# Performance work log

Measured on AMD Instinct MI355X. Metric: run time of the kernel, lower is better.

## Reference

```python
import jax, jax.numpy as jnp
import numpy as np

NH = 12      # bert-base heads
NL = 32      # num_latents
K = 64       # hard-coded topk in forward


def _ln(x, g, b):
    m = x.mean(-1, keepdims=True)
    v = ((x - m) ** 2).mean(-1, keepdims=True)
    return (x - m) / jnp.sqrt(v + 1e-12) * g + b


def _attn(xq, xkv, w, b, mask_add=None):
    # w: [4,H,H] (q,k,v,o), b: [4,H]
    B, Lq, H = xq.shape
    dh = H // NH
    q = (xq @ w[0] + b[0]).reshape(B, Lq, NH, dh)
    k = (xkv @ w[1] + b[1]).reshape(B, -1, NH, dh)
    v = (xkv @ w[2] + b[2]).reshape(B, -1, NH, dh)
    s = jnp.einsum('bqhd,bkhd->bhqk', q, k) / np.sqrt(dh).astype(xq.dtype)
    if mask_add is not None:
        s = s + mask_add
    p = jax.nn.softmax(s, axis=-1)          # [B,NH,Lq,Lk]
    o = jnp.einsum('bhqk,bkhd->bqhd', p, v).reshape(B, Lq, H)
    return o @ w[3] + b[3], p


def _cross_block(q, enc, w, b, g, lb, mask_add=None):
    # w:[L,8,H,H]; per layer: self-attn+LN then cross-attn+LN (FFN stripped)
    p_last = None
    for l in range(w.shape[0]):
        a, _ = _attn(q, q, w[l, :4], b[l, :4])
        q = _ln(q + a, g[l, 0], lb[l, 0])
        a, p_last = _attn(q, enc, w[l, 4:], b[l, 4:], mask_add)
        q = _ln(q + a, g[l, 1], lb[l, 1])
    return q, p_last


def _self_block(q, w, b, g, lb):
    probs = []
    for l in range(w.shape[0]):
        a, p = _attn(q, q, w[l], b[l])
        q = _ln(q + a, g[l, 0], lb[l, 0])
        probs.append(p)
    return q, jnp.concatenate(probs, axis=1)  # concat over head dim like torch.concat(attentions, dim=1)


def setup_inputs() -> dict:
    key = jax.random.key(0)
    ks = jax.random.split(key, 24)
    B, S, T, H, L = 32, 1024, 64, 768, 2
    std = 0.02
    inp = {
        'audio_embeds': jax.random.normal(ks[0], (B, S, H), jnp.float32),
        'text_embeds': jax.random.normal(ks[1], (B, T, H), jnp.float32),
        'attention_mask': jnp.ones((B, T), jnp.int32),
        'audio_qt': jax.random.normal(ks[2], (1, NL, H), jnp.float32) * std,
        'text_qt': jax.random.normal(ks[3], (1, NL, H), jnp.float32) * std,
    }
    for i, pre in enumerate(['tm', 'am', 'mg']):
        inp[pre + '_w'] = jax.random.normal(ks[4 + i], (L, 8, H, H), jnp.float32) * std
        inp[pre + '_b'] = jnp.zeros((L, 8, H), jnp.float32)
        inp[pre + '_g'] = jnp.ones((L, 2, H), jnp.float32)
        inp[pre + '_lb'] = jnp.zeros((L, 2, H), jnp.float32)
    inp['sel_w'] = jax.random.normal(ks[8], (L, 4, H, H), jnp.float32) * std
    inp['sel_b'] = jnp.zeros((L, 4, H), jnp.float32)
    inp['sel_g'] = jnp.ones((L, 1, H), jnp.float32)
    inp['sel_lb'] = jnp.zeros((L, 1, H), jnp.float32)
    return inp


def reference(audio_embeds, text_embeds, audio_qt, text_qt,
              tm_w, tm_b, tm_g, tm_lb, am_w, am_b, am_g, am_lb,
              sel_w, sel_b, sel_g, sel_lb, mg_w, mg_b, mg_g, mg_lb,
              attention_mask):
    B, S, H = audio_embeds.shape
    mask_add = (1.0 - attention_mask.astype(audio_embeds.dtype))[:, None, None, :] * -1e4

    # text token merger
    latent_text, _ = _cross_block(jnp.broadcast_to(text_qt, (B, NL, H)), text_embeds,
                                  tm_w, tm_b, tm_g, tm_lb, mask_add)
    # audio token merger (capture last-layer cross-attn probs)
    latent_audio, cross_p = _cross_block(jnp.broadcast_to(audio_qt, (B, NL, H)), audio_embeds,
                                         am_w, am_b, am_g, am_lb)
    latent_attention_score = cross_p.mean(axis=1)          # [B,NL,S]

    latent = jnp.concatenate([latent_audio, latent_text], axis=1)  # [B,2NL,H]
    fused, attn_all = _self_block(latent, sel_w, sel_b, sel_g, sel_lb)  # attn_all [B,L*NH,2NL,2NL]
    aas = attn_all[:, :, :NL, NL:].mean(axis=1)            # [B,NL,NL]

    imp = jnp.einsum('bqk,bks->bqs', aas, latent_attention_score).mean(axis=1)  # [B,S]
    _, idx = jax.lax.top_k(imp, K)
    sorted_idx = jnp.sort(idx, axis=1)                     # [B,K]

    sel_mask = jnp.zeros((B, S), bool).at[jnp.arange(B)[:, None], sorted_idx].set(True)
    q_tokens = jnp.take_along_axis(audio_embeds, sorted_idx[..., None], axis=1)  # [B,K,H]
    unsel_idx = jnp.argsort(sel_mask, axis=1, stable=True)[:, :S - K]            # order-preserving
    kv_rest = jnp.take_along_axis(audio_embeds, unsel_idx[..., None], axis=1)    # [B,S-K,H]
    kv = jnp.concatenate([kv_rest, fused], axis=1)                               # [B,S,H]

    out, _ = _cross_block(q_tokens, kv, mg_w, mg_b, mg_g, mg_lb)
    return out
```

## Files before the change

### kernel.cpp

```cpp
#include <hip/hip_runtime.h>
#include <hip/hip_bf16.h>
#include <math.h>

namespace {
constexpr int kB = 32, kS = 1024, kT = 64, kH = 768, kNH = 12, kDH = 64;
constexpr int kNL = 32, kTopK = 64, kL = 2;
constexpr size_t kMat = (size_t)kH * kH;
}

typedef _Float16 half8 __attribute__((ext_vector_type(8)));
typedef float floatx4 __attribute__((ext_vector_type(4)));

#define AS1U(p) ((const __attribute__((address_space(1))) unsigned int*)(p))
#define AS3U(p) ((__attribute__((address_space(3))) unsigned int*)(p))

__device__ __forceinline__ void split_write(float v, _Float16* H, _Float16* L, size_t i) {
    _Float16 h = (_Float16)v;
    H[i] = h;
    L[i] = (_Float16)(v - (float)h);
}

template<int NP>
__global__ __launch_bounds__(256) void gemm16(
    const _Float16* __restrict__ Aqh, const _Float16* __restrict__ Aql,
    const _Float16* __restrict__ Aeh, const _Float16* __restrict__ Ael,
    const _Float16* __restrict__ Whb, const _Float16* __restrict__ Wlb,
    const float* __restrict__ bias,
    _Float16* __restrict__ O0h, _Float16* __restrict__ O0l,
    _Float16* __restrict__ O1h, _Float16* __restrict__ O1l,
    _Float16* __restrict__ O2h, _Float16* __restrict__ O2l,
    int Mq, int Mk)
{
    const int z = blockIdx.z;
    const int M = (z == 0) ? Mq : Mk;
    if ((int)blockIdx.x * 128 >= M) return;
    const _Float16* Ah = (z == 0) ? Aqh : Aeh;
    const _Float16* Al = (z == 0) ? Aql : Ael;
    const _Float16* Bh = Whb + (size_t)z * kMat;
    const _Float16* Bl = Wlb + (size_t)z * kMat;
    const float* bz = bias + z * kH;
    _Float16* Oh = (z == 0) ? O0h : (z == 1) ? O1h : O2h;
    _Float16* Ol = (z == 0) ? O0l : (z == 1) ? O1l : O2l;

    constexpr int NPL = (NP == 3) ? 4 : 2;
    __shared__ _Float16 lds[NPL * 4096];
    const int tid = threadIdx.x;
    const int lane = tid & 63, wave = tid >> 6;
    const size_t rm = (size_t)blockIdx.x * 128;
    const size_t cn = (size_t)blockIdx.y * 128;
    const int wr = (wave >> 1) * 64, wc = (wave & 1) * 64;

    const int lrow = lane >> 2;
    const int lchunk = (lane & 3) ^ ((lane >> 3) & 3);
    const int q = lane >> 4;
    const int fr = lane & 15;
    const int rslot = q ^ ((fr >> 1) & 3);

    const _Float16* gsrc;
    _Float16* lbase;
    int jbase;
    if constexpr (NP == 3) {
        gsrc = (wave == 0) ? Ah + rm * kH : (wave == 1) ? Al + rm * kH
             : (wave == 2) ? Bh + cn * kH : Bl + cn * kH;
        lbase = &lds[wave * 4096];
        jbase = 0;
    } else {
        gsrc = (wave < 2) ? Ah + rm * kH : Bh + cn * kH;
        lbase = &lds[(wave >> 1) * 4096];
        jbase = (wave & 1) * 4;
    }
    constexpr int CPW = (NP == 3) ? 8 : 4;

    floatx4 acc[4][4] = {};

    for (int k0 = 0; k0 < kH; k0 += 32) {
        #pragma unroll
        for (int c = 0; c < CPW; ++c) {
            int j = jbase + c;
            const _Float16* src = gsrc + (size_t)(j * 16 + lrow) * kH + k0 + lchunk * 8;
            _Float16* dst = lbase + j * 512 + lane * 8;
            __builtin_amdgcn_global_load_lds(AS1U(src), AS3U(dst), 16, 0, 0);
        }
        __syncthreads();

        half8 ah[4], bh[4], al[4], bl[4];
        #pragma unroll
        for (int m = 0; m < 4; ++m) {
            int r = wr + m * 16 + fr;
            ah[m] = *(const half8*)&lds[r * 32 + rslot * 8];
            if constexpr (NP == 3) al[m] = *(const half8*)&lds[4096 + r * 32 + rslot * 8];
        }
        constexpr int pb = (NP == 3) ? 2 : 1;
        #pragma unroll
        for (int n = 0; n < 4; ++n) {
            int r = wc + n * 16 + fr;
            bh[n] = *(const half8*)&lds[pb * 4096 + r * 32 + rslot * 8];
            if constexpr (NP == 3) bl[n] = *(const half8*)&lds[3 * 4096 + r * 32 + rslot * 8];
        }
        #pragma unroll
        for (int m = 0; m < 4; ++m)
            #pragma unroll
            for (int n = 0; n < 4; ++n) {
                acc[m][n] = __builtin_amdgcn_mfma_f32_16x16x32_f16(ah[m], bh[n], acc[m][n], 0, 0, 0);
                if constexpr (NP == 3) {
                    acc[m][n] = __builtin_amdgcn_mfma_f32_16x16x32_f16(ah[m], bl[n], acc[m][n], 0, 0, 0);
                    acc[m][n] = __builtin_amdgcn_mfma_f32_16x16x32_f16(al[m], bh[n], acc[m][n], 0, 0, 0);
                }
            }
        __syncthreads();
    }
    #pragma unroll
    for (int m = 0; m < 4; ++m) {
        int row0 = wr + m * 16 + (lane >> 4) * 4;
        #pragma unroll
        for (int n = 0; n < 4; ++n) {
            int col = (int)cn + wc + n * 16 + fr;
            float bv = bz[col];
            #pragma unroll
            for (int j = 0; j < 4; ++j) {
                float v = acc[m][n][j] + bv;
                size_t oi = (rm + row0 + j) * (size_t)kH + col;
                _Float16 hh = (_Float16)v;
                Oh[oi] = hh;
                if constexpr (NP == 3) Ol[oi] = (_Float16)(v - (float)hh);
            }
        }
    }
}

template<int NP>
__global__ __launch_bounds__(256) void gemm16s(
    const _Float16* __restrict__ Aqh, const _Float16* __restrict__ Aql,
    const _Float16* __restrict__ Aeh, const _Float16* __restrict__ Ael,
    const _Float16* __restrict__ Whb, const _Float16* __restrict__ Wlb,
    const float* __restrict__ bias,
    _Float16* __restrict__ O0h, _Float16* __restrict__ O0l,
    _Float16* __restrict__ O1h, _Float16* __restrict__ O1l,
    _Float16* __restrict__ O2h, _Float16* __restrict__ O2l,
    int Mq, int Mk)
{
    const int z = blockIdx.z;
    const int M = (z == 0) ? Mq : Mk;
    if ((int)blockIdx.x * 64 >= M) return;
    const _Float16* Ah = (z == 0) ? Aqh : Aeh;
    const _Float16* Al = (z == 0) ? Aql : Ael;
    const _Float16* Bh = Whb + (size_t)z * kMat;
    const _Float16* Bl = Wlb + (size_t)z * kMat;
    const float* bz = bias + z * kH;
    _Float16* Oh = (z == 0) ? O0h : (z == 1) ? O1h : O2h;
    _Float16* Ol = (z == 0) ? O0l : (z == 1) ? O1l : O2l;

    constexpr int NPL = (NP == 3) ? 4 : 2;
    __shared__ _Float16 lds[NPL * 2048];
    const int tid = threadIdx.x;
    const int lane = tid & 63, wave = tid >> 6;
    const size_t rm = (size_t)blockIdx.x * 64;
    const size_t cn = (size_t)blockIdx.y * 64;
    const int wr = (wave >> 1) * 32, wc = (wave & 1) * 32;

    const int lrow = lane >> 2;
    const int lchunk = (lane & 3) ^ ((lane >> 3) & 3);
    const int q = lane >> 4;
    const int fr = lane & 15;
    const int rslot = q ^ ((fr >> 1) & 3);

    const _Float16* gsrc;
    _Float16* lbase;
    int jbase;
    if constexpr (NP == 3) {
        gsrc = (wave == 0) ? Ah + rm * kH : (wave == 1) ? Al + rm * kH
             : (wave == 2) ? Bh + cn * kH : Bl + cn * kH;
        lbase = &lds[wave * 2048];
        jbase = 0;
    } else {
        gsrc = (wave < 2) ? Ah + rm * kH : Bh + cn * kH;
        lbase = &lds[(wave >> 1) * 2048];
        jbase = (wave & 1) * 2;
    }
    constexpr int CPW = (NP == 3) ? 4 : 2;

    floatx4 acc[2][2] = {};

    for (int k0 = 0; k0 < kH; k0 += 32) {
        #pragma unroll
        for (int c = 0; c < CPW; ++c) {
            int j = jbase + c;
            const _Float16* src = gsrc + (size_t)(j * 16 + lrow) * kH + k0 + lchunk * 8;
            _Float16* dst = lbase + j * 512 + lane * 8;
            __builtin_amdgcn_global_load_lds(AS1U(src), AS3U(dst), 16, 0, 0);
        }
        __syncthreads();

        half8 ah[2], bh[2], al[2], bl[2];
        #pragma unroll
        for (int m = 0; m < 2; ++m) {
            int r = wr + m * 16 + fr;
            ah[m] = *(const half8*)&lds[r * 32 + rslot * 8];
            if constexpr (NP == 3) al[m] = *(const half8*)&lds[2048 + r * 32 + rslot * 8];
        }
        constexpr int pb = (NP == 3) ? 2 : 1;
        #pragma unroll
        for (int n = 0; n < 2; ++n) {
            int r = wc + n * 16 + fr;
            bh[n] = *(const half8*)&lds[pb * 2048 + r * 32 + rslot * 8];
            if constexpr (NP == 3) bl[n] = *(const half8*)&lds[3 * 2048 + r * 32 + rslot * 8];
        }
        #pragma unroll
        for (int m = 0; m < 2; ++m)
            #pragma unroll
            for (int n = 0; n < 2; ++n) {
                acc[m][n] = __builtin_amdgcn_mfma_f32_16x16x32_f16(ah[m], bh[n], acc[m][n], 0, 0, 0);
                if constexpr (NP == 3) {
                    acc[m][n] = __builtin_amdgcn_mfma_f32_16x16x32_f16(ah[m], bl[n], acc[m][n], 0, 0, 0);
                    acc[m][n] = __builtin_amdgcn_mfma_f32_16x16x32_f16(al[m], bh[n], acc[m][n], 0, 0, 0);
                }
            }
        __syncthreads();
    }
    #pragma unroll
    for (int m = 0; m < 2; ++m) {
        int row0 = wr + m * 16 + (lane >> 4) * 4;
        #pragma unroll
        for (int n = 0; n < 2; ++n) {
            int col = (int)cn + wc + n * 16 + fr;
            float bv = bz[col];
            #pragma unroll
            for (int j = 0; j < 4; ++j) {
                float v = acc[m][n][j] + bv;
                size_t oi = (rm + row0 + j) * (size_t)kH + col;
                _Float16 hh = (_Float16)v;
                Oh[oi] = hh;
                if constexpr (NP == 3) Ol[oi] = (_Float16)(v - (float)hh);
            }
        }
    }
}

template<int NP>
__global__ __launch_bounds__(256) void gemm_o32s(
    const _Float16* __restrict__ Ah_, const _Float16* __restrict__ Al_,
    const _Float16* __restrict__ Bh_, const _Float16* __restrict__ Bl_,
    const float* __restrict__ bias, float* __restrict__ Y, int M)
{
    constexpr int NPL = (NP == 3) ? 4 : 2;
    __shared__ _Float16 lds[NPL * 2048];
    const int tid = threadIdx.x;
    const int lane = tid & 63, wave = tid >> 6;
    const size_t rm = (size_t)blockIdx.x * 64;
    const size_t cn = (size_t)blockIdx.y * 64;
    const int wr = (wave >> 1) * 32, wc = (wave & 1) * 32;

    const int lrow = lane >> 2;
    const int lchunk = (lane & 3) ^ ((lane >> 3) & 3);
    const int q = lane >> 4;
    const int fr = lane & 15;
    const int rslot = q ^ ((fr >> 1) & 3);

    const _Float16* gsrc;
    _Float16* lbase;
    int jbase;
    if constexpr (NP == 3) {
        gsrc = (wave == 0) ? Ah_ + rm * kH : (wave == 1) ? Al_ + rm * kH
             : (wave == 2) ? Bh_ + cn * kH : Bl_ + cn * kH;
        lbase = &lds[wave * 2048];
        jbase = 0;
    } else {
        gsrc = (wave < 2) ? Ah_ + rm * kH : Bh_ + cn * kH;
        lbase = &lds[(wave >> 1) * 2048];
        jbase = (wave & 1) * 2;
    }
    constexpr int CPW = (NP == 3) ? 4 : 2;

    floatx4 acc[2][2] = {};
    for (int k0 = 0; k0 < kH; k0 += 32) {
        #pragma unroll
        for (int c = 0; c < CPW; ++c) {
            int j = jbase + c;
            const _Float16* src = gsrc + (size_t)(j * 16 + lrow) * kH + k0 + lchunk * 8;
            _Float16* dst = lbase + j * 512 + lane * 8;
            __builtin_amdgcn_global_load_lds(AS1U(src), AS3U(dst), 16, 0, 0);
        }
        __syncthreads();
        half8 ah[2], bh[2], al[2], bl[2];
        #pragma unroll
        for (int m = 0; m < 2; ++m) {
            int r = wr + m * 16 + fr;
            ah[m] = *(const half8*)&lds[r * 32 + rslot * 8];
            if constexpr (NP == 3) al[m] = *(const half8*)&lds[2048 + r * 32 + rslot * 8];
        }
        constexpr int pb = (NP == 3) ? 2 : 1;
        #pragma unroll
        for (int n = 0; n < 2; ++n) {
            int r = wc + n * 16 + fr;
            bh[n] = *(const half8*)&lds[pb * 2048 + r * 32 + rslot * 8];
            if constexpr (NP == 3) bl[n] = *(const half8*)&lds[3 * 2048 + r * 32 + rslot * 8];
        }
        #pragma unroll
        for (int m = 0; m < 2; ++m)
            #pragma unroll
            for (int n = 0; n < 2; ++n) {
                acc[m][n] = __builtin_amdgcn_mfma_f32_16x16x32_f16(ah[m], bh[n], acc[m][n], 0, 0, 0);
                if constexpr (NP == 3) {
                    acc[m][n] = __builtin_amdgcn_mfma_f32_16x16x32_f16(ah[m], bl[n], acc[m][n], 0, 0, 0);
                    acc[m][n] = __builtin_amdgcn_mfma_f32_16x16x32_f16(al[m], bh[n], acc[m][n], 0, 0, 0);
                }
            }
        __syncthreads();
    }
    #pragma unroll
    for (int m = 0; m < 2; ++m) {
        int row0 = wr + m * 16 + (lane >> 4) * 4;
        #pragma unroll
        for (int n = 0; n < 2; ++n) {
            int col = (int)cn + wc + n * 16 + fr;
            float bv = bias[col];
            #pragma unroll
            for (int j = 0; j < 4; ++j)
                Y[(rm + row0 + j) * (size_t)kH + col] = acc[m][n][j] + bv;
        }
    }
}

template<int NP>
__global__ __launch_bounds__(256) void attn_big(
    const _Float16* __restrict__ Qh, const _Float16* __restrict__ Ql,
    const _Float16* __restrict__ Kh, const _Float16* __restrict__ Kl,
    float* __restrict__ P, int Lq, int Lk)
{
    constexpr int NPL = (NP == 3) ? 2 : 1;
    const int tid = threadIdx.x, lane = tid & 63, wave = tid >> 6;
    const int fr = lane & 15, part = lane >> 4;
    const int bh = blockIdx.x, b = bh / kNH, h = bh % kNH;
    const int q0 = blockIdx.y * 32;
    const int key0 = wave * 256;
    __shared__ float red[32][4];

    half8 qa[2][2][NPL];
    #pragma unroll
    for (int m = 0; m < 2; ++m)
        #pragma unroll
        for (int c = 0; c < 2; ++c) {
            size_t ro = (size_t)(b * Lq + q0 + m * 16 + fr) * kH + h * kDH + c * 32 + part * 8;
            qa[m][c][0] = *(const half8*)&Qh[ro];
            if constexpr (NP == 3) qa[m][c][1] = *(const half8*)&Ql[ro];
        }
    floatx4 acc[2][16] = {};
    #pragma unroll
    for (int n = 0; n < 16; ++n)
        #pragma unroll
        for (int c = 0; c < 2; ++c) {
            size_t ro = (size_t)(b * Lk + key0 + n * 16 + fr) * kH + h * kDH + c * 32 + part * 8;
            half8 kh8 = *(const half8*)&Kh[ro];
            half8 kl8;
            if constexpr (NP == 3) kl8 = *(const half8*)&Kl[ro];
            #pragma unroll
            for (int m = 0; m < 2; ++m) {
                acc[m][n] = __builtin_amdgcn_mfma_f32_16x16x32_f16(qa[m][c][0], kh8, acc[m][n], 0, 0, 0);
                if constexpr (NP == 3) {
                    acc[m][n] = __builtin_amdgcn_mfma_f32_16x16x32_f16(qa[m][c][0], kl8, acc[m][n], 0, 0, 0);
                    acc[m][n] = __builtin_amdgcn_mfma_f32_16x16x32_f16(qa[m][c][1], kh8, acc[m][n], 0, 0, 0);
                }
            }
        }
    #pragma unroll
    for (int m = 0; m < 2; ++m)
        #pragma unroll
        for (int n = 0; n < 16; ++n)
            #pragma unroll
            for (int j = 0; j < 4; ++j) acc[m][n][j] *= 0.125f;
    #pragma unroll
    for (int m = 0; m < 2; ++m)
        #pragma unroll
        for (int j = 0; j < 4; ++j) {
            float v = acc[m][0][j];
            #pragma unroll
            for (int n = 1; n < 16; ++n) v = fmaxf(v, acc[m][n][j]);
            #pragma unroll
            for (int o = 1; o < 16; o <<= 1) v = fmaxf(v, __shfl_xor(v, o));
            red[m * 16 + part * 4 + j][wave] = v;
        }
    __syncthreads();
    float gm[2][4];
    #pragma unroll
    for (int m = 0; m < 2; ++m)
        #pragma unroll
        for (int j = 0; j < 4; ++j) {
            int r = m * 16 + part * 4 + j;
            gm[m][j] = fmaxf(fmaxf(red[r][0], red[r][1]), fmaxf(red[r][2], red[r][3]));
        }
    __syncthreads();
    #pragma unroll
    for (int m = 0; m < 2; ++m)
        #pragma unroll
        for (int j = 0; j < 4; ++j) {
            float s = 0.f;
            #pragma unroll
            for (int n = 0; n < 16; ++n) {
                float e = expf(acc[m][n][j] - gm[m][j]);
                acc[m][n][j] = e;
                s += e;
            }
            #pragma unroll
            for (int o = 1; o < 16; o <<= 1) s += __shfl_xor(s, o);
            red[m * 16 + part * 4 + j][wave] = s;
        }
    __syncthreads();
    #pragma unroll
    for (int m = 0; m < 2; ++m)
        #pragma unroll
        for (int j = 0; j < 4; ++j) {
            int r = m * 16 + part * 4 + j;
            float inv = 1.0f / (red[r][0] + red[r][1] + red[r][2] + red[r][3]);
            size_t rowbase = ((size_t)bh * Lq + q0 + m * 16 + part * 4 + j) * Lk + key0;
            #pragma unroll
            for (int n = 0; n < 16; ++n)
                P[rowbase + n * 16 + fr] = acc[m][n][j] * inv;
        }
}

template<int LQ, int NP>
__global__ __launch_bounds__((LQ / 16) * 64) void pv_mfma(
    const float* __restrict__ P,
    const _Float16* __restrict__ Vh, const _Float16* __restrict__ Vl,
    _Float16* __restrict__ Oh, _Float16* __restrict__ Ol, int Lk)
{
    constexpr int NW = LQ / 16, NT = NW * 64;
    constexpr int NPL = (NP == 3) ? 2 : 1;
    __shared__ _Float16 vT[NPL][64][72];
    const int tid = threadIdx.x, lane = tid & 63, wave = tid >> 6;
    const int fr = lane & 15, part = lane >> 4;
    const int bh = blockIdx.x, b = bh / kNH, h = bh % kNH;
    const int qbase = wave * 16;

    floatx4 acc[4] = {};
    for (int kb = 0; kb < Lk; kb += 64) {
        for (int idx = tid; idx < 64 * 8; idx += NT) {
            int r = idx >> 3, c8 = idx & 7;
            half8 v = *(const half8*)&Vh[(size_t)(b * Lk + kb + r) * kH + h * kDH + c8 * 8];
            #pragma unroll
            for (int e = 0; e < 8; ++e) vT[0][c8 * 8 + e][r] = v[e];
            if constexpr (NP == 3) {
                half8 w = *(const half8*)&Vl[(size_t)(b * Lk + kb + r) * kH + h * kDH + c8 * 8];
                #pragma unroll
                for (int e = 0; e < 8; ++e) vT[1][c8 * 8 + e][r] = w[e];
            }
        }
        __syncthreads();
        half8 pa[2][NPL];
        #pragma unroll
        for (int c = 0; c < 2; ++c) {
            const float* src = &P[((size_t)bh * LQ + qbase + fr) * Lk + kb + c * 32 + part * 8];
            float4 x = *(const float4*)src, y = *(const float4*)(src + 4);
            float vv[8] = {x.x, x.y, x.z, x.w, y.x, y.y, y.z, y.w};
            #pragma unroll
            for (int e = 0; e < 8; ++e) {
                _Float16 hh = (_Float16)vv[e];
                pa[c][0][e] = hh;
                if constexpr (NP == 3) pa[c][1][e] = (_Float16)(vv[e] - (float)hh);
            }
        }
        #pragma unroll
        for (int n = 0; n < 4; ++n)
            #pragma unroll
            for (int c = 0; c < 2; ++c) {
                half8 bh8 = *(const half8*)&vT[0][n * 16 + fr][c * 32 + part * 8];
                acc[n] = __builtin_amdgcn_mfma_f32_16x16x32_f16(pa[c][0], bh8, acc[n], 0, 0, 0);
                if constexpr (NP == 3) {
                    half8 bl8 = *(const half8*)&vT[1][n * 16 + fr][c * 32 + part * 8];
                    acc[n] = __builtin_amdgcn_mfma_f32_16x16x32_f16(pa[c][0], bl8, acc[n], 0, 0, 0);
                    acc[n] = __builtin_amdgcn_mfma_f32_16x16x32_f16(pa[c][1], bh8, acc[n], 0, 0, 0);
                }
            }
        __syncthreads();
    }
    #pragma unroll
    for (int n = 0; n < 4; ++n)
        #pragma unroll
        for (int j = 0; j < 4; ++j) {
            size_t oi = (size_t)(b * LQ + qbase + part * 4 + j) * kH + h * kDH + n * 16 + fr;
            float v = acc[n][j];
            _Float16 hh = (_Float16)v;
            Oh[oi] = hh;
            if constexpr (NP == 3) Ol[oi] = (_Float16)(v - (float)hh);
        }
}

template<int LQ, int LK, int NP, bool MASKED, bool CAPTURE>
__global__ __launch_bounds__((LQ / 16) * 64) void attn_small(
    const _Float16* Qh, const _Float16* Ql,
    const _Float16* __restrict__ Kh, const _Float16* __restrict__ Kl,
    const _Float16* __restrict__ Vh, const _Float16* __restrict__ Vl,
    _Float16* Oh, _Float16* Ol,
    float* __restrict__ Pcap, const int* __restrict__ amask)
{
    constexpr int NW = LQ / 16, NT = NW * 64, NN = LK / 16, NC = LK / 32;
    constexpr int NPL = (NP == 3) ? 2 : 1;
    constexpr int PIT = LK + 8;
    __shared__ _Float16 vT[NPL][64][PIT];
    __shared__ _Float16 Pld[NW][NPL][16][PIT];
    const int tid = threadIdx.x, lane = tid & 63, wave = tid >> 6;
    const int fr = lane & 15, part = lane >> 4;
    const int bh = blockIdx.x, b = bh / kNH, h = bh % kNH;

    for (int idx = tid; idx < LK * 8; idx += NT) {
        int r = idx >> 3, c8 = idx & 7;
        half8 v = *(const half8*)&Vh[(size_t)(b * LK + r) * kH + h * kDH + c8 * 8];
        #pragma unroll
        for (int e = 0; e < 8; ++e) vT[0][c8 * 8 + e][r] = v[e];
        if constexpr (NP == 3) {
            half8 w = *(const half8*)&Vl[(size_t)(b * LK + r) * kH + h * kDH + c8 * 8];
            #pragma unroll
            for (int e = 0; e < 8; ++e) vT[1][c8 * 8 + e][r] = w[e];
        }
    }
    half8 qa[2][NPL];
    #pragma unroll
    for (int c = 0; c < 2; ++c) {
        size_t ro = (size_t)(b * LQ + wave * 16 + fr) * kH + h * kDH + c * 32 + part * 8;
        qa[c][0] = *(const half8*)&Qh[ro];
        if constexpr (NP == 3) qa[c][1] = *(const half8*)&Ql[ro];
    }
    floatx4 acc[NN] = {};
    #pragma unroll
    for (int n = 0; n < NN; ++n)
        #pragma unroll
        for (int c = 0; c < 2; ++c) {
            size_t ro = (size_t)(b * LK + n * 16 + fr) * kH + h * kDH + c * 32 + part * 8;
            half8 kh8 = *(const half8*)&Kh[ro];
            acc[n] = __builtin_amdgcn_mfma_f32_16x16x32_f16(qa[c][0], kh8, acc[n], 0, 0, 0);
            if constexpr (NP == 3) {
                half8 kl8 = *(const half8*)&Kl[ro];
                acc[n] = __builtin_amdgcn_mfma_f32_16x16x32_f16(qa[c][0], kl8, acc[n], 0, 0, 0);
                acc[n] = __builtin_amdgcn_mfma_f32_16x16x32_f16(qa[c][1], kh8, acc[n], 0, 0, 0);
            }
        }
    #pragma unroll
    for (int n = 0; n < NN; ++n) {
        float madd = 0.f;
        if constexpr (MASKED)
            madd = (1.0f - (float)amask[b * kT + n * 16 + fr]) * -1e4f;
        #pragma unroll
        for (int j = 0; j < 4; ++j) acc[n][j] = acc[n][j] * 0.125f + madd;
    }
    #pragma unroll
    for (int j = 0; j < 4; ++j) {
        float m = acc[0][j];
        #pragma unroll
        for (int n = 1; n < NN; ++n) m = fmaxf(m, acc[n][j]);
        #pragma unroll
        for (int o = 1; o < 16; o <<= 1) m = fmaxf(m, __shfl_xor(m, o));
        float s = 0.f;
        #pragma unroll
        for (int n = 0; n < NN; ++n) { float e = expf(acc[n][j] - m); acc[n][j] = e; s += e; }
        #pragma unroll
        for (int o = 1; o < 16; o <<= 1) s += __shfl_xor(s, o);
        float inv = 1.0f / s;
        #pragma unroll
        for (int n = 0; n < NN; ++n) acc[n][j] *= inv;
    }
    #pragma unroll
    for (int n = 0; n < NN; ++n)
        #pragma unroll
        for (int j = 0; j < 4; ++j) {
            float p = acc[n][j];
            if constexpr (CAPTURE)
                Pcap[((size_t)bh * LQ + wave * 16 + part * 4 + j) * LK + n * 16 + fr] = p;
            _Float16 ph = (_Float16)p;
            Pld[wave][0][part * 4 + j][n * 16 + fr] = ph;
            if constexpr (NP == 3)
                Pld[wave][1][part * 4 + j][n * 16 + fr] = (_Float16)(p - (float)ph);
        }
    __syncthreads();
    floatx4 o4[4] = {};
    #pragma unroll
    for (int n = 0; n < 4; ++n)
        #pragma unroll
        for (int c = 0; c < NC; ++c) {
            half8 ph8 = *(const half8*)&Pld[wave][0][fr][c * 32 + part * 8];
            half8 vh8 = *(const half8*)&vT[0][n * 16 + fr][c * 32 + part * 8];
            o4[n] = __builtin_amdgcn_mfma_f32_16x16x32_f16(ph8, vh8, o4[n], 0, 0, 0);
            if constexpr (NP == 3) {
                half8 pl8 = *(const half8*)&Pld[wave][1][fr][c * 32 + part * 8];
                half8 vl8 = *(const half8*)&vT[1][n * 16 + fr][c * 32 + part * 8];
                o4[n] = __builtin_amdgcn_mfma_f32_16x16x32_f16(ph8, vl8, o4[n], 0, 0, 0);
                o4[n] = __builtin_amdgcn_mfma_f32_16x16x32_f16(pl8, vh8, o4[n], 0, 0, 0);
            }
        }
    #pragma unroll
    for (int n = 0; n < 4; ++n)
        #pragma unroll
        for (int j = 0; j < 4; ++j) {
            size_t oi = (size_t)(b * LQ + wave * 16 + part * 4 + j) * kH + h * kDH + n * 16 + fr;
            float v = o4[n][j];
            _Float16 hh = (_Float16)v;
            Oh[oi] = hh;
            if constexpr (NP == 3) Ol[oi] = (_Float16)(v - (float)hh);
        }
}

__global__ __launch_bounds__(256) void wconv(const float* __restrict__ W,
    _Float16* __restrict__ Th, _Float16* __restrict__ Tl)
{
    __shared__ float t[32][33];
    const int mat = blockIdx.z;
    const int k0 = blockIdx.y * 32, n0 = blockIdx.x * 32;
    const int tid = threadIdx.x;
    #pragma unroll
    for (int i = 0; i < 4; ++i) {
        int e = tid + i * 256, r = e >> 5, c = e & 31;
        t[r][c] = W[(size_t)mat * kMat + (size_t)(k0 + r) * kH + n0 + c];
    }
    __syncthreads();
    #pragma unroll
    for (int i = 0; i < 4; ++i) {
        int e = tid + i * 256, r = e >> 5, c = e & 31;
        float v = t[c][r];
        split_write(v, Th, Tl, (size_t)mat * kMat + (size_t)(n0 + r) * kH + k0 + c);
    }
}

__global__ __launch_bounds__(256) void split2(const float* __restrict__ X,
    _Float16* __restrict__ H, _Float16* __restrict__ L, int n)
{
    int i = (blockIdx.x * 256 + threadIdx.x) * 4;
    if (i >= n) return;
    float4 v = *(const float4*)&X[i];
    split_write(v.x, H, L, i);
    split_write(v.y, H, L, i + 1);
    split_write(v.z, H, L, i + 2);
    split_write(v.w, H, L, i + 3);
}

__global__ __launch_bounds__(256) void ln_residual(const float* __restrict__ X,
    const float* __restrict__ A, const float* __restrict__ g,
    const float* __restrict__ lb, float* __restrict__ Y,
    _Float16* __restrict__ Yh, _Float16* __restrict__ Yl)
{
    const size_t row = blockIdx.x;
    const int tid = threadIdx.x;
    __shared__ float red[4];
    float x[3];
    float sum = 0.f;
    #pragma unroll
    for (int i = 0; i < 3; ++i) {
        int c = tid + i * 256;
        x[i] = X[row * kH + c] + A[row * kH + c];
        sum += x[i];
    }
    for (int o = 32; o > 0; o >>= 1) sum += __shfl_xor(sum, o);
    if ((tid & 63) == 0) red[tid >> 6] = sum;
    __syncthreads();
    sum = red[0] + red[1] + red[2] + red[3];
    float mean = sum * (1.0f / 768.0f);
    float vs = 0.f;
    #pragma unroll
    for (int i = 0; i < 3; ++i) { float d = x[i] - mean; vs += d * d; }
    for (int o = 32; o > 0; o >>= 1) vs += __shfl_xor(vs, o);
    __syncthreads();
    if ((tid & 63) == 0) red[tid >> 6] = vs;
    __syncthreads();
    vs = red[0] + red[1] + red[2] + red[3];
    float inv = 1.0f / sqrtf(vs * (1.0f / 768.0f) + 1e-12f);
    #pragma unroll
    for (int i = 0; i < 3; ++i) {
        int c = tid + i * 256;
        float y = (x[i] - mean) * inv * g[c] + lb[c];
        Y[row * kH + c] = y;
        if (Yh) split_write(y, Yh, Yl, row * kH + c);
    }
}

__global__ __launch_bounds__(256) void mean_heads(const float* __restrict__ P,
    float* __restrict__ out)
{
    const int bq = blockIdx.x;
    const int b = bq / kNL, q = bq % kNL;
    for (int s = threadIdx.x; s < kS; s += 256) {
        float acc = 0.f;
        for (int h = 0; h < kNH; ++h)
            acc += P[((size_t)(b * kNH + h) * kNL + q) * kS + s];
        out[(size_t)bq * kS + s] = acc * (1.0f / kNH);
    }
}

__global__ __launch_bounds__(256) void aas_acc(const float* __restrict__ P,
    float* __restrict__ aas, int init)
{
    const int b = blockIdx.x;
    for (int idx = threadIdx.x; idx < kNL * kNL; idx += 256) {
        int q = idx >> 5, k = idx & 31;
        float acc = 0.f;
        for (int h = 0; h < kNH; ++h)
            acc += P[((size_t)(b * kNH + h) * 64 + q) * 64 + 32 + k];
        size_t o = (size_t)b * kNL * kNL + idx;
        if (init) aas[o] = acc; else aas[o] += acc;
    }
}

__global__ __launch_bounds__(256) void imp_kernel(const float* __restrict__ aas,
    const float* __restrict__ score, float* __restrict__ imp)
{
    const int b = blockIdx.x;
    __shared__ float w[kNL];
    if (threadIdx.x < kNL) {
        float acc = 0.f;
        for (int q = 0; q < kNL; ++q)
            acc += aas[((size_t)b * kNL + q) * kNL + threadIdx.x];
        w[threadIdx.x] = acc;
    }
    __syncthreads();
    for (int s = threadIdx.x; s < kS; s += 256) {
        float acc = 0.f;
        for (int k = 0; k < kNL; ++k)
            acc += w[k] * score[((size_t)b * kNL + k) * kS + s];
        imp[(size_t)b * kS + s] = acc;
    }
}

__global__ __launch_bounds__(256) void topk_kernel(const float* __restrict__ imp,
    int* __restrict__ selidx, int* __restrict__ unselidx)
{
    const int b = blockIdx.x;
    const int tid = threadIdx.x;
    __shared__ unsigned long long keys[kS];
    __shared__ int wsum[4];
    for (int i = tid; i < kS; i += 256) {
        unsigned u = __float_as_uint(imp[(size_t)b * kS + i]);
        u = (u & 0x80000000u) ? ~u : (u | 0x80000000u);
        keys[i] = ((unsigned long long)u << 32) | (unsigned)(kS - 1 - i);
    }
    __syncthreads();
    unsigned long long me[4];
    int r[4] = {0, 0, 0, 0};
    #pragma unroll
    for (int j = 0; j < 4; ++j) me[j] = keys[tid * 4 + j];
    for (int t = 0; t < kS; ++t) {
        unsigned long long k = keys[t];
        #pragma unroll
        for (int j = 0; j < 4; ++j) r[j] += (k > me[j]) ? 1 : 0;
    }
    int flag[4], cnt = 0;
    #pragma unroll
    for (int j = 0; j < 4; ++j) { flag[j] = (r[j] < kTopK); cnt += flag[j]; }
    const int lane = tid & 63, w = tid >> 6;
    int incl = cnt;
    for (int o = 1; o < 64; o <<= 1) {
        int t = __shfl_up(incl, o);
        if (lane >= o) incl += t;
    }
    if (lane == 63) wsum[w] = incl;
    __syncthreads();
    int wbase = 0;
    for (int i = 0; i < w; ++i) wbase += wsum[i];
    int sbase = wbase + incl - cnt;
    int ubase = tid * 4 - sbase;
    #pragma unroll
    for (int j = 0; j < 4; ++j) {
        int i = tid * 4 + j;
        if (flag[j]) selidx[b * kTopK + sbase++] = i;
        else         unselidx[b * (kS - kTopK) + ubase++] = i;
    }
}

__global__ __launch_bounds__(256) void bcast_q(const float* __restrict__ qt,
    float* __restrict__ q, _Float16* __restrict__ Qh, _Float16* __restrict__ Ql)
{
    const int bn = blockIdx.x;
    const int n = bn & (kNL - 1);
    for (int c = threadIdx.x; c < kH; c += 256) {
        float v = qt[(size_t)n * kH + c];
        q[(size_t)bn * kH + c] = v;
        split_write(v, Qh, Ql, (size_t)bn * kH + c);
    }
}

__global__ __launch_bounds__(256) void concat_lat(const float* __restrict__ qa,
    const float* __restrict__ qt, float* __restrict__ lat,
    _Float16* __restrict__ Lh, _Float16* __restrict__ Ll)
{
    const int br = blockIdx.x;
    const int b = br >> 6, r = br & 63;
    const float* src = (r < kNL) ? qa + (size_t)(b * kNL + r) * kH
                                 : qt + (size_t)(b * kNL + (r - kNL)) * kH;
    for (int c = threadIdx.x; c < kH; c += 256) {
        float v = src[c];
        lat[(size_t)br * kH + c] = v;
        split_write(v, Lh, Ll, (size_t)br * kH + c);
    }
}

__global__ __launch_bounds__(256) void gather_q(const float* __restrict__ audio,
    const int* __restrict__ selidx, float* __restrict__ qm,
    _Float16* __restrict__ Qh, _Float16* __restrict__ Ql)
{
    const int bj = blockIdx.x;
    const int b = bj >> 6;
    const int srow = selidx[bj];
    const float* src = audio + ((size_t)b * kS + srow) * kH;
    for (int c = threadIdx.x; c < kH; c += 256) {
        float v = src[c];
        qm[(size_t)bj * kH + c] = v;
        split_write(v, Qh, Ql, (size_t)bj * kH + c);
    }
}

__global__ __launch_bounds__(256) void build_kv(const float* __restrict__ audio,
    const float* __restrict__ fused, const int* __restrict__ unselidx,
    _Float16* __restrict__ Kh, _Float16* __restrict__ Kl)
{
    const int br = blockIdx.x;
    const int b = br >> 10, r = br & 1023;
    const float* src;
    if (r < kS - kTopK) src = audio + ((size_t)b * kS + unselidx[b * (kS - kTopK) + r]) * kH;
    else                src = fused + (size_t)(b * kTopK + (r - (kS - kTopK))) * kH;
    for (int c = threadIdx.x; c < kH; c += 256)
        split_write(src[c], Kh, Kl, (size_t)br * kH + c);
}

extern "C" void kernel_launch(void* const* d_in, const int* in_sizes, int n_in,
                              void* d_out, int out_size, void* d_ws, size_t ws_size,
                              hipStream_t stream)
{
    const float* audio    = (const float*)d_in[0];
    const float* text     = (const float*)d_in[1];
    const int*   amask    = (const int*)  d_in[2];
    const float* audio_qt = (const float*)d_in[3];
    const float* text_qt  = (const float*)d_in[4];
    const float* tm_w  = (const float*)d_in[5];
    const float* tm_b  = (const float*)d_in[6];
    const float* tm_g  = (const float*)d_in[7];
    const float* tm_lb = (const float*)d_in[8];
    const float* am_w  = (const float*)d_in[9];
    const float* am_b  = (const float*)d_in[10];
    const float* am_g  = (const float*)d_in[11];
    const float* am_lb = (const float*)d_in[12];
    const float* mg_w  = (const float*)d_in[13];
    const float* mg_b  = (const float*)d_in[14];
    const float* mg_g  = (const float*)d_in[15];
    const float* mg_lb = (const float*)d_in[16];
    const float* sel_w  = (const float*)d_in[17];
    const float* sel_b  = (const float*)d_in[18];
    const float* sel_g  = (const float*)d_in[19];
    const float* sel_lb = (const float*)d_in[20];
    (void)in_sizes; (void)n_in; (void)out_size;

    char* base = (char*)d_ws;
    size_t off = 0;
    auto alloc = [&](size_t bytes) {
        off = (off + 255) & ~(size_t)255;
        void* p = base + off; off += bytes; return p;
    };
    float* Pbuf   = (float*)alloc((size_t)kB * kNH * 64 * kS * 4);
    float* attA   = (float*)alloc((size_t)2048 * kH * 4);
    float* q_text = (float*)alloc((size_t)1024 * kH * 4);
    float* q_audio= (float*)alloc((size_t)1024 * kH * 4);
    float* latent = (float*)alloc((size_t)2048 * kH * 4);
    float* qmerge = (float*)alloc((size_t)2048 * kH * 4);
    float* latsc  = (float*)alloc((size_t)kB * kNL * kS * 4);
    float* aas    = (float*)alloc((size_t)kB * kNL * kNL * 4);
    float* impb   = (float*)alloc((size_t)kB * kS * 4);
    int* selidx   = (int*)alloc((size_t)kB * kTopK * 4);
    int* unselidx = (int*)alloc((size_t)kB * (kS - kTopK) * 4);
    _Float16* Wh  = (_Float16*)alloc(16 * kMat * 2);
    _Float16* Wl  = (_Float16*)alloc(16 * kMat * 2);
    _Float16* BGh = (_Float16*)alloc((size_t)kB * kS * kH * 2);
    _Float16* BGl = (_Float16*)alloc((size_t)kB * kS * kH * 2);
    _Float16* PTh = (_Float16*)alloc((size_t)kB * kT * kH * 2);
    _Float16* PTl = (_Float16*)alloc((size_t)kB * kT * kH * 2);
    _Float16* PLqh= (_Float16*)alloc((size_t)2048 * kH * 2);
    _Float16* PLql= (_Float16*)alloc((size_t)2048 * kH * 2);
    _Float16* PLoh= (_Float16*)alloc((size_t)2048 * kH * 2);
    _Float16* PLol= (_Float16*)alloc((size_t)2048 * kH * 2);
    _Float16* KVh = (_Float16*)alloc((size_t)kB * kS * kH * 2);
    _Float16* KVl = (_Float16*)alloc((size_t)kB * kS * kH * 2);
    if (off > ws_size) return;

    _Float16* Qh = PLoh;
    _Float16* Ql = PLol;

    auto attn = [&](const float* qf, int Lq,
                    const _Float16* qah, const _Float16* qal,
                    const _Float16* eah, const _Float16* eal, int Lk,
                    int wmat, const float* bias, const float* g, const float* lb,
                    const int* mask, int capture, bool np3,
                    float* q_out, _Float16* oh, _Float16* ol)
    {
        const int Mq = kB * Lq, Mk = kB * Lk;
        const _Float16* WhB = Wh + (size_t)wmat * kMat;
        const _Float16* WlB = Wl + (size_t)wmat * kMat;
        if (Lk >= 256) {
            const int gx = Mk / 128;
            dim3 g1(gx, 6, 2);
            if (np3) gemm16<3><<<g1, 256, 0, stream>>>(qah, qal, eah, eal, WhB, WlB, bias,
                         Qh, Ql, KVh, KVl, nullptr, nullptr, Mq, Mk);
            else     gemm16<1><<<g1, 256, 0, stream>>>(qah, qal, eah, eal, WhB, WlB, bias,
                         Qh, Ql, KVh, KVl, nullptr, nullptr, Mq, Mk);
            dim3 g2(kB * kNH, Lq / 32);
            if (np3) attn_big<3><<<g2, 256, 0, stream>>>(Qh, Ql, KVh, KVl, Pbuf, Lq, Lk);
            else     attn_big<1><<<g2, 256, 0, stream>>>(Qh, Ql, KVh, KVl, Pbuf, Lq, Lk);
            if (capture == 1) mean_heads<<<kB * kNL, 256, 0, stream>>>(Pbuf, latsc);
            dim3 g3(Mk / 128, 6, 1);
            if (np3) gemm16<3><<<g3, 256, 0, stream>>>(eah, eal, eah, eal,
                         WhB + 2 * kMat, WlB + 2 * kMat, bias + 2 * kH,
                         KVh, KVl, nullptr, nullptr, nullptr, nullptr, Mk, Mk);
            else     gemm16<1><<<g3, 256, 0, stream>>>(eah, eal, eah, eal,
                         WhB + 2 * kMat, WlB + 2 * kMat, bias + 2 * kH,
                         KVh, KVl, nullptr, nullptr, nullptr, nullptr, Mk, Mk);
            if (Lq == 32) {
                if (np3) pv_mfma<32, 3><<<kB * kNH, 128, 0, stream>>>(Pbuf, KVh, KVl, PLoh, PLol, Lk);
                else     pv_mfma<32, 1><<<kB * kNH, 128, 0, stream>>>(Pbuf, KVh, KVl, PLoh, PLol, Lk);
            } else {
                if (np3) pv_mfma<64, 3><<<kB * kNH, 256, 0, stream>>>(Pbuf, KVh, KVl, PLoh, PLol, Lk);
                else     pv_mfma<64, 1><<<kB * kNH, 256, 0, stream>>>(Pbuf, KVh, KVl, PLoh, PLol, Lk);
            }
        } else {
            _Float16* V2h = KVh + (size_t)Mk * kH;
            _Float16* V2l = KVl + (size_t)Mk * kH;
            const int gx = (Mq > Mk ? Mq : Mk) / 64;
            dim3 g1(gx, 12, 3);
            if (np3) gemm16s<3><<<g1, 256, 0, stream>>>(qah, qal, eah, eal, WhB, WlB, bias,
                         Qh, Ql, KVh, KVl, V2h, V2l, Mq, Mk);
            else     gemm16s<1><<<g1, 256, 0, stream>>>(qah, qal, eah, eal, WhB, WlB, bias,
                         Qh, Ql, KVh, KVl, V2h, V2l, Mq, Mk);
            if (Lq == 32 && Lk == 32)
                attn_small<32, 32, 3, false, false><<<kB * kNH, 128, 0, stream>>>(
                    Qh, Ql, KVh, KVl, V2h, V2l, PLoh, PLol, nullptr, nullptr);
            else if (Lq == 32 && Lk == 64)
                attn_small<32, 64, 3, true, false><<<kB * kNH, 128, 0, stream>>>(
                    Qh, Ql, KVh, KVl, V2h, V2l, PLoh, PLol, nullptr, mask);
            else if (np3)
                attn_small<64, 64, 3, false, true><<<kB * kNH, 256, 0, stream>>>(
                    Qh, Ql, KVh, KVl, V2h, V2l, PLoh, PLol, Pbuf, nullptr);
            else
                attn_small<64, 64, 1, false, false><<<kB * kNH, 256, 0, stream>>>(
                    Qh, Ql, KVh, KVl, V2h, V2l, PLoh, PLol, nullptr, nullptr);
            if (capture == 2)      aas_acc<<<kB, 256, 0, stream>>>(Pbuf, aas, 1);
            else if (capture == 3) aas_acc<<<kB, 256, 0, stream>>>(Pbuf, aas, 0);
        }
        dim3 g4(Mq / 64, 12);
        if (np3) gemm_o32s<3><<<g4, 256, 0, stream>>>(PLoh, PLol, WhB + 3 * kMat, WlB + 3 * kMat,
                     bias + 3 * kH, attA, Mq);
        else     gemm_o32s<1><<<g4, 256, 0, stream>>>(PLoh, PLol, WhB + 3 * kMat, WlB + 3 * kMat,
                     bias + 3 * kH, attA, Mq);
        ln_residual<<<Mq, 256, 0, stream>>>(qf, attA, g, lb, q_out, oh, ol);
    };

    split2<<<(kB * kT * kH) / 1024, 256, 0, stream>>>(text, PTh, PTl, kB * kT * kH);
    split2<<<(kB * kS * kH) / 1024, 256, 0, stream>>>(audio, BGh, BGl, kB * kS * kH);

    wconv<<<dim3(24, 24, 16), 256, 0, stream>>>(tm_w, Wh, Wl);
    bcast_q<<<kB * kNL, 256, 0, stream>>>(text_qt, q_text, PLqh, PLql);
    for (int l = 0; l < kL; ++l) {
        attn(q_text, kNL, PLqh, PLql, PLqh, PLql, kNL, l * 8 + 0,
             tm_b + (size_t)l * 8 * kH, tm_g + (size_t)l * 2 * kH, tm_lb + (size_t)l * 2 * kH,
             nullptr, 0, true, q_text, PLqh, PLql);
        attn(q_text, kNL, PLqh, PLql, PTh, PTl, kT, l * 8 + 4,
             tm_b + ((size_t)l * 8 + 4) * kH, tm_g + ((size_t)l * 2 + 1) * kH, tm_lb + ((size_t)l * 2 + 1) * kH,
             amask, 0, true, q_text, PLqh, PLql);
    }
    wconv<<<dim3(24, 24, 16), 256, 0, stream>>>(am_w, Wh, Wl);
    bcast_q<<<kB * kNL, 256, 0, stream>>>(audio_qt, q_audio, PLqh, PLql);
    for (int l = 0; l < kL; ++l) {
        attn(q_audio, kNL, PLqh, PLql, PLqh, PLql, kNL, l * 8 + 0,
             am_b + (size_t)l * 8 * kH, am_g + (size_t)l * 2 * kH, am_lb + (size_t)l * 2 * kH,
             nullptr, 0, true, q_audio, PLqh, PLql);
        attn(q_audio, kNL, PLqh, PLql, BGh, BGl, kS, l * 8 + 4,
             am_b + ((size_t)l * 8 + 4) * kH, am_g + ((size_t)l * 2 + 1) * kH, am_lb + ((size_t)l * 2 + 1) * kH,
             nullptr, (l == kL - 1) ? 1 : 0, true, q_audio, PLqh, PLql);
    }
    concat_lat<<<kB * 64, 256, 0, stream>>>(q_audio, q_text, latent, PLqh, PLql);
    wconv<<<dim3(24, 24, 8), 256, 0, stream>>>(sel_w, Wh, Wl);
    for (int l = 0; l < kL; ++l) {
        attn(latent, 64, PLqh, PLql, PLqh, PLql, 64, l * 4,
             sel_b + (size_t)l * 4 * kH, sel_g + (size_t)l * kH, sel_lb + (size_t)l * kH,
             nullptr, (l == 0) ? 2 : 3, true, latent, PLqh, PLql);
    }
    imp_kernel<<<kB, 256, 0, stream>>>(aas, latsc, impb);
    topk_kernel<<<kB, 256, 0, stream>>>(impb, selidx, unselidx);
    gather_q<<<kB * kTopK, 256, 0, stream>>>(audio, selidx, qmerge, PLqh, PLql);
    build_kv<<<kB * kS, 256, 0, stream>>>(audio, latent, unselidx, BGh, BGl);
    wconv<<<dim3(24, 24, 16), 256, 0, stream>>>(mg_w, Wh, Wl);
    for (int l = 0; l < kL; ++l) {
        attn(qmerge, 64, PLqh, PLql, PLqh, PLql, 64, l * 8 + 0,
             mg_b + (size_t)l * 8 * kH, mg_g + (size_t)l * 2 * kH, mg_lb + (size_t)l * 2 * kH,
             nullptr, 0, false, qmerge, PLqh, PLql);
        float* qo = (l == kL - 1) ? (float*)d_out : qmerge;
        _Float16* oh = (l == kL - 1) ? nullptr : PLqh;
        _Float16* ol = (l == kL - 1) ? nullptr : PLql;
        attn(qmerge, 64, PLqh, PLql, BGh, BGl, kS, l * 8 + 4,
             mg_b + ((size_t)l * 8 + 4) * kH, mg_g + ((size_t)l * 2 + 1) * kH, mg_lb + ((size_t)l * 2 + 1) * kH,
             nullptr, 0, false, qo, oh, ol);
    }
}
```

Measured before the change: 2.107 ms.

## Swizzle large K/V GEMM grid, split Q projection, convert weights per layer

Replaces the 3D-grid combined Q/K projection GEMM with a separate small-tile Q GEMM and a 1D-grid K/V GEMM. The new grid uses an XCD-aware block swizzle, so the tiles that share A rows stay together on one die's L2. Weight conversion to split fp16 now runs per layer into a half-size buffer instead of per block. This shrinks the workspace and may improve L2 locality, at the cost of extra kernel launches.

```diff
diff --git a/kernel.cpp b/kernel.cpp
--- a/kernel.cpp
+++ b/kernel.cpp
@@ -21,33 +21,26 @@
 }
 
 template<int NP>
-__global__ __launch_bounds__(256) void gemm16(
-    const _Float16* __restrict__ Aqh, const _Float16* __restrict__ Aql,
-    const _Float16* __restrict__ Aeh, const _Float16* __restrict__ Ael,
-    const _Float16* __restrict__ Whb, const _Float16* __restrict__ Wlb,
+__global__ __launch_bounds__(256) void gemm16x(
+    const _Float16* __restrict__ Ah_, const _Float16* __restrict__ Al_,
+    const _Float16* __restrict__ Bh_, const _Float16* __restrict__ Bl_,
     const float* __restrict__ bias,
-    _Float16* __restrict__ O0h, _Float16* __restrict__ O0l,
-    _Float16* __restrict__ O1h, _Float16* __restrict__ O1l,
-    _Float16* __restrict__ O2h, _Float16* __restrict__ O2l,
-    int Mq, int Mk)
-{
-    const int z = blockIdx.z;
-    const int M = (z == 0) ? Mq : Mk;
-    if ((int)blockIdx.x * 128 >= M) return;
-    const _Float16* Ah = (z == 0) ? Aqh : Aeh;
-    const _Float16* Al = (z == 0) ? Aql : Ael;
-    const _Float16* Bh = Whb + (size_t)z * kMat;
-    const _Float16* Bl = Wlb + (size_t)z * kMat;
-    const float* bz = bias + z * kH;
-    _Float16* Oh = (z == 0) ? O0h : (z == 1) ? O1h : O2h;
-    _Float16* Ol = (z == 0) ? O0l : (z == 1) ? O1l : O2l;
+    _Float16* __restrict__ Oh, _Float16* __restrict__ Ol, int M)
+{
+    const int nwg = gridDim.x;
+    const int bid = blockIdx.x;
+    const int cpx = nwg >> 3;
+    const int swz = (bid & 7) * cpx + (bid >> 3);
+    const int xn = swz % 6;
+    const int ym = swz / 6;
+    if (ym * 128 >= M) return;
 
     constexpr int NPL = (NP == 3) ? 4 : 2;
     __shared__ _Float16 lds[NPL * 4096];
     const int tid = threadIdx.x;
     const int lane = tid & 63, wave = tid >> 6;
-    const size_t rm = (size_t)blockIdx.x * 128;
-    const size_t cn = (size_t)blockIdx.y * 128;
+    const size_t rm = (size_t)ym * 128;
+    const size_t cn = (size_t)xn * 128;
     const int wr = (wave >> 1) * 64, wc = (wave & 1) * 64;
 
     const int lrow = lane >> 2;
@@ -60,19 +53,18 @@
     _Float16* lbase;
     int jbase;
     if constexpr (NP == 3) {
-        gsrc = (wave == 0) ? Ah + rm * kH : (wave == 1) ? Al + rm * kH
-             : (wave == 2) ? Bh + cn * kH : Bl + cn * kH;
+        gsrc = (wave == 0) ? Ah_ + rm * kH : (wave == 1) ? Al_ + rm * kH
+             : (wave == 2) ? Bh_ + cn * kH : Bl_ + cn * kH;
         lbase = &lds[wave * 4096];
         jbase = 0;
     } else {
-        gsrc = (wave < 2) ? Ah + rm * kH : Bh + cn * kH;
+        gsrc = (wave < 2) ? Ah_ + rm * kH : Bh_ + cn * kH;
         lbase = &lds[(wave >> 1) * 4096];
         jbase = (wave & 1) * 4;
     }
     constexpr int CPW = (NP == 3) ? 8 : 4;
 
     floatx4 acc[4][4] = {};
-
     for (int k0 = 0; k0 < kH; k0 += 32) {
         #pragma unroll
         for (int c = 0; c < CPW; ++c) {
@@ -82,7 +74,6 @@
             __builtin_amdgcn_global_load_lds(AS1U(src), AS3U(dst), 16, 0, 0);
         }
         __syncthreads();
-
         half8 ah[4], bh[4], al[4], bl[4];
         #pragma unroll
         for (int m = 0; m < 4; ++m) {
@@ -115,7 +106,7 @@
         #pragma unroll
         for (int n = 0; n < 4; ++n) {
             int col = (int)cn + wc + n * 16 + fr;
-            float bv = bz[col];
+            float bv = bias[col];
             #pragma unroll
             for (int j = 0; j < 4; ++j) {
                 float v = acc[m][n][j] + bv;
@@ -180,7 +171,6 @@
     constexpr int CPW = (NP == 3) ? 4 : 2;
 
     floatx4 acc[2][2] = {};
-
     for (int k0 = 0; k0 < kH; k0 += 32) {
         #pragma unroll
         for (int c = 0; c < CPW; ++c) {
@@ -190,7 +180,6 @@
             __builtin_amdgcn_global_load_lds(AS1U(src), AS3U(dst), 16, 0, 0);
         }
         __syncthreads();
-
         half8 ah[2], bh[2], al[2], bl[2];
         #pragma unroll
         for (int m = 0; m < 2; ++m) {
@@ -846,33 +835,33 @@
 
     char* base = (char*)d_ws;
     size_t off = 0;
-    auto alloc = [&](size_t bytes) {
+    auto A = [&](size_t bytes) {
         off = (off + 255) & ~(size_t)255;
         void* p = base + off; off += bytes; return p;
     };
-    float* Pbuf   = (float*)alloc((size_t)kB * kNH * 64 * kS * 4);
-    float* attA   = (float*)alloc((size_t)2048 * kH * 4);
-    float* q_text = (float*)alloc((size_t)1024 * kH * 4);
-    float* q_audio= (float*)alloc((size_t)1024 * kH * 4);
-    float* latent = (float*)alloc((size_t)2048 * kH * 4);
-    float* qmerge = (float*)alloc((size_t)2048 * kH * 4);
-    float* latsc  = (float*)alloc((size_t)kB * kNL * kS * 4);
-    float* aas    = (float*)alloc((size_t)kB * kNL * kNL * 4);
-    float* impb   = (float*)alloc((size_t)kB * kS * 4);
-    int* selidx   = (int*)alloc((size_t)kB * kTopK * 4);
-    int* unselidx = (int*)alloc((size_t)kB * (kS - kTopK) * 4);
-    _Float16* Wh  = (_Float16*)alloc(16 * kMat * 2);
-    _Float16* Wl  = (_Float16*)alloc(16 * kMat * 2);
-    _Float16* BGh = (_Float16*)alloc((size_t)kB * kS * kH * 2);
-    _Float16* BGl = (_Float16*)alloc((size_t)kB * kS * kH * 2);
-    _Float16* PTh = (_Float16*)alloc((size_t)kB * kT * kH * 2);
-    _Float16* PTl = (_Float16*)alloc((size_t)kB * kT * kH * 2);
-    _Float16* PLqh= (_Float16*)alloc((size_t)2048 * kH * 2);
-    _Float16* PLql= (_Float16*)alloc((size_t)2048 * kH * 2);
-    _Float16* PLoh= (_Float16*)alloc((size_t)2048 * kH * 2);
-    _Float16* PLol= (_Float16*)alloc((size_t)2048 * kH * 2);
-    _Float16* KVh = (_Float16*)alloc((size_t)kB * kS * kH * 2);
-    _Float16* KVl = (_Float16*)alloc((size_t)kB * kS * kH * 2);
+    float* Pbuf   = (float*)A((size_t)kB * kNH * 64 * kS * 4);
+    float* attA   = (float*)A((size_t)2048 * kH * 4);
+    float* q_text = (float*)A((size_t)1024 * kH * 4);
+    float* q_audio= (float*)A((size_t)1024 * kH * 4);
+    float* latent = (float*)A((size_t)2048 * kH * 4);
+    float* qmerge = (float*)A((size_t)2048 * kH * 4);
+    float* latsc  = (float*)A((size_t)kB * kNL * kS * 4);
+    float* aas    = (float*)A((size_t)kB * kNL * kNL * 4);
+    float* impb   = (float*)A((size_t)kB * kS * 4);
+    int* selidx   = (int*)A((size_t)kB * kTopK * 4);
+    int* unselidx = (int*)A((size_t)kB * (kS - kTopK) * 4);
+    _Float16* Wh  = (_Float16*)A(8 * kMat * 2);
+    _Float16* Wl  = (_Float16*)A(8 * kMat * 2);
+    _Float16* BGh = (_Float16*)A((size_t)kB * kS * kH * 2);
+    _Float16* BGl = (_Float16*)A((size_t)kB * kS * kH * 2);
+    _Float16* PTh = (_Float16*)A((size_t)kB * kT * kH * 2);
+    _Float16* PTl = (_Float16*)A((size_t)kB * kT * kH * 2);
+    _Float16* PLqh= (_Float16*)A((size_t)2048 * kH * 2);
+    _Float16* PLql= (_Float16*)A((size_t)2048 * kH * 2);
+    _Float16* PLoh= (_Float16*)A((size_t)2048 * kH * 2);
+    _Float16* PLol= (_Float16*)A((size_t)2048 * kH * 2);
+    _Float16* KVh = (_Float16*)A((size_t)kB * kS * kH * 2);
+    _Float16* KVl = (_Float16*)A((size_t)kB * kS * kH * 2);
     if (off > ws_size) return;
 
     _Float16* Qh = PLoh;
@@ -889,23 +878,24 @@
         const _Float16* WhB = Wh + (size_t)wmat * kMat;
         const _Float16* WlB = Wl + (size_t)wmat * kMat;
         if (Lk >= 256) {
-            const int gx = Mk / 128;
-            dim3 g1(gx, 6, 2);
-            if (np3) gemm16<3><<<g1, 256, 0, stream>>>(qah, qal, eah, eal, WhB, WlB, bias,
-                         Qh, Ql, KVh, KVl, nullptr, nullptr, Mq, Mk);
-            else     gemm16<1><<<g1, 256, 0, stream>>>(qah, qal, eah, eal, WhB, WlB, bias,
-                         Qh, Ql, KVh, KVl, nullptr, nullptr, Mq, Mk);
+            dim3 gq(Mq / 64, 12, 1);
+            if (np3) gemm16s<3><<<gq, 256, 0, stream>>>(qah, qal, qah, qal, WhB, WlB, bias,
+                         Qh, Ql, nullptr, nullptr, nullptr, nullptr, Mq, Mq);
+            else     gemm16s<1><<<gq, 256, 0, stream>>>(qah, qal, qah, qal, WhB, WlB, bias,
+                         Qh, Ql, nullptr, nullptr, nullptr, nullptr, Mq, Mq);
+            const int nwgK = 6 * (Mk / 128);
+            if (np3) gemm16x<3><<<nwgK, 256, 0, stream>>>(eah, eal, WhB + 1 * kMat, WlB + 1 * kMat,
+                         bias + 1 * kH, KVh, KVl, Mk);
+            else     gemm16x<1><<<nwgK, 256, 0, stream>>>(eah, eal, WhB + 1 * kMat, WlB + 1 * kMat,
+                         bias + 1 * kH, KVh, KVl, Mk);
             dim3 g2(kB * kNH, Lq / 32);
             if (np3) attn_big<3><<<g2, 256, 0, stream>>>(Qh, Ql, KVh, KVl, Pbuf, Lq, Lk);
             else     attn_big<1><<<g2, 256, 0, stream>>>(Qh, Ql, KVh, KVl, Pbuf, Lq, Lk);
             if (capture == 1) mean_heads<<<kB * kNL, 256, 0, stream>>>(Pbuf, latsc);
-            dim3 g3(Mk / 128, 6, 1);
-            if (np3) gemm16<3><<<g3, 256, 0, stream>>>(eah, eal, eah, eal,
-                         WhB + 2 * kMat, WlB + 2 * kMat, bias + 2 * kH,
-                         KVh, KVl, nullptr, nullptr, nullptr, nullptr, Mk, Mk);
-            else     gemm16<1><<<g3, 256, 0, stream>>>(eah, eal, eah, eal,
-                         WhB + 2 * kMat, WlB + 2 * kMat, bias + 2 * kH,
-                         KVh, KVl, nullptr, nullptr, nullptr, nullptr, Mk, Mk);
+            if (np3) gemm16x<3><<<nwgK, 256, 0, stream>>>(eah, eal, WhB + 2 * kMat, WlB + 2 * kMat,
+                         bias + 2 * kH, KVh, KVl, Mk);
+            else     gemm16x<1><<<nwgK, 256, 0, stream>>>(eah, eal, WhB + 2 * kMat, WlB + 2 * kMat,
+                         bias + 2 * kH, KVh, KVl, Mk);
             if (Lq == 32) {
                 if (np3) pv_mfma<32, 3><<<kB * kNH, 128, 0, stream>>>(Pbuf, KVh, KVl, PLoh, PLol, Lk);
                 else     pv_mfma<32, 1><<<kB * kNH, 128, 0, stream>>>(Pbuf, KVh, KVl, PLoh, PLol, Lk);
@@ -948,30 +938,30 @@
     split2<<<(kB * kT * kH) / 1024, 256, 0, stream>>>(text, PTh, PTl, kB * kT * kH);
     split2<<<(kB * kS * kH) / 1024, 256, 0, stream>>>(audio, BGh, BGl, kB * kS * kH);
 
-    wconv<<<dim3(24, 24, 16), 256, 0, stream>>>(tm_w, Wh, Wl);
     bcast_q<<<kB * kNL, 256, 0, stream>>>(text_qt, q_text, PLqh, PLql);
     for (int l = 0; l < kL; ++l) {
-        attn(q_text, kNL, PLqh, PLql, PLqh, PLql, kNL, l * 8 + 0,
+        wconv<<<dim3(24, 24, 8), 256, 0, stream>>>(tm_w + (size_t)l * 8 * kMat, Wh, Wl);
+        attn(q_text, kNL, PLqh, PLql, PLqh, PLql, kNL, 0,
              tm_b + (size_t)l * 8 * kH, tm_g + (size_t)l * 2 * kH, tm_lb + (size_t)l * 2 * kH,
              nullptr, 0, true, q_text, PLqh, PLql);
-        attn(q_text, kNL, PLqh, PLql, PTh, PTl, kT, l * 8 + 4,
+        attn(q_text, kNL, PLqh, PLql, PTh, PTl, kT, 4,
              tm_b + ((size_t)l * 8 + 4) * kH, tm_g + ((size_t)l * 2 + 1) * kH, tm_lb + ((size_t)l * 2 + 1) * kH,
              amask, 0, true, q_text, PLqh, PLql);
     }
-    wconv<<<dim3(24, 24, 16), 256, 0, stream>>>(am_w, Wh, Wl);
     bcast_q<<<kB * kNL, 256, 0, stream>>>(audio_qt, q_audio, PLqh, PLql);
     for (int l = 0; l < kL; ++l) {
-        attn(q_audio, kNL, PLqh, PLql, PLqh, PLql, kNL, l * 8 + 0,
+        wconv<<<dim3(24, 24, 8), 256, 0, stream>>>(am_w + (size_t)l * 8 * kMat, Wh, Wl);
+        attn(q_audio, kNL, PLqh, PLql, PLqh, PLql, kNL, 0,
              am_b + (size_t)l * 8 * kH, am_g + (size_t)l * 2 * kH, am_lb + (size_t)l * 2 * kH,
              nullptr, 0, true, q_audio, PLqh, PLql);
-        attn(q_audio, kNL, PLqh, PLql, BGh, BGl, kS, l * 8 + 4,
+        attn(q_audio, kNL, PLqh, PLql, BGh, BGl, kS, 4,
              am_b + ((size_t)l * 8 + 4) * kH, am_g + ((size_t)l * 2 + 1) * kH, am_lb + ((size_t)l * 2 + 1) * kH,
              nullptr, (l == kL - 1) ? 1 : 0, true, q_audio, PLqh, PLql);
     }
     concat_lat<<<kB * 64, 256, 0, stream>>>(q_audio, q_text, latent, PLqh, PLql);
-    wconv<<<dim3(24, 24, 8), 256, 0, stream>>>(sel_w, Wh, Wl);
     for (int l = 0; l < kL; ++l) {
-        attn(latent, 64, PLqh, PLql, PLqh, PLql, 64, l * 4,
+        wconv<<<dim3(24, 24, 4), 256, 0, stream>>>(sel_w + (size_t)l * 4 * kMat, Wh, Wl);
+        attn(latent, 64, PLqh, PLql, PLqh, PLql, 64, 0,
              sel_b + (size_t)l * 4 * kH, sel_g + (size_t)l * kH, sel_lb + (size_t)l * kH,
              nullptr, (l == 0) ? 2 : 3, true, latent, PLqh, PLql);
     }
@@ -979,15 +969,15 @@
     topk_kernel<<<kB, 256, 0, stream>>>(impb, selidx, unselidx);
     gather_q<<<kB * kTopK, 256, 0, stream>>>(audio, selidx, qmerge, PLqh, PLql);
     build_kv<<<kB * kS, 256, 0, stream>>>(audio, latent, unselidx, BGh, BGl);
-    wconv<<<dim3(24, 24, 16), 256, 0, stream>>>(mg_w, Wh, Wl);
     for (int l = 0; l < kL; ++l) {
-        attn(qmerge, 64, PLqh, PLql, PLqh, PLql, 64, l * 8 + 0,
+        wconv<<<dim3(24, 24, 8), 256, 0, stream>>>(mg_w + (size_t)l * 8 * kMat, Wh, Wl);
+        attn(qmerge, 64, PLqh, PLql, PLqh, PLql, 64, 0,
              mg_b + (size_t)l * 8 * kH, mg_g + (size_t)l * 2 * kH, mg_lb + (size_t)l * 2 * kH,
              nullptr, 0, false, qmerge, PLqh, PLql);
         float* qo = (l == kL - 1) ? (float*)d_out : qmerge;
         _Float16* oh = (l == kL - 1) ? nullptr : PLqh;
         _Float16* ol = (l == kL - 1) ? nullptr : PLql;
-        attn(qmerge, 64, PLqh, PLql, BGh, BGl, kS, l * 8 + 4,
+        attn(qmerge, 64, PLqh, PLql, BGh, BGl, kS, 4,
              mg_b + ((size_t)l * 8 + 4) * kH, mg_g + ((size_t)l * 2 + 1) * kH, mg_lb + ((size_t)l * 2 + 1) * kH,
              nullptr, 0, false, qo, oh, ol);
     }
```

Measured after the change: 2.088 ms. About the same (-0.9%).
